# Kernel optimization log

Measured on AMD Instinct MI355X. Metric: run time of the kernel, lower is better.

## Reference

```python
import jax, jax.numpy as jnp
import numpy as np

B, N, DOP, DM, H = 8, 2048, 256, 256, 256  # batch, n_ops==n_machines, dims


def setup_inputs() -> dict:
    key = jax.random.key(0)
    ks = jax.random.split(key, 21)
    s = 0.02
    inp = {
        "operation_features": jax.random.normal(ks[0], (B, N, DOP), jnp.float32),
        "machine_features": jax.random.normal(ks[1], (B, N, DM), jnp.float32),
        "type_match_mask": jax.random.bernoulli(ks[2], 0.3, (B, N, N)).astype(jnp.float32),
        "same_type_mask": jax.random.bernoulli(ks[3], 0.3, (B, N, N)).astype(jnp.float32),
        "oma_q_w": jax.random.normal(ks[4], (H, DM), jnp.float32) * s,
        "oma_q_b": jnp.zeros((H,), jnp.float32),
        "oma_kv_w": jax.random.normal(ks[5], (2 * H, DOP), jnp.float32) * s,
        "oma_kv_b": jnp.zeros((2 * H,), jnp.float32),
        "oma_s_w": jax.random.normal(ks[6], (1, 2 * H), jnp.float32) * s,
        "oma_s_b": jnp.zeros((1,), jnp.float32),
        "oma_o_w": jax.random.normal(ks[7], (DM, H), jnp.float32) * s,
        "oma_o_b": jnp.zeros((DM,), jnp.float32),
        "sa_w_w": jax.random.normal(ks[8], (3 * H, DM), jnp.float32) * s,
        "sa_w_b": jnp.zeros((3 * H,), jnp.float32),
        "sa_s_w": jax.random.normal(ks[9], (1, 2 * H), jnp.float32) * s,
        "sa_s_b": jnp.zeros((1,), jnp.float32),
        "sa_o_w": jax.random.normal(ks[10], (DM, H), jnp.float32) * s,
        "sa_o_b": jnp.zeros((DM,), jnp.float32),
        "mix_w": jax.random.normal(ks[11], (DM, 2 * DM), jnp.float32) * s,
        "mix_b": jnp.zeros((DM,), jnp.float32),
    }
    return inp


def reference(operation_features, machine_features, type_match_mask, same_type_mask,
              oma_q_w, oma_q_b, oma_kv_w, oma_kv_b, oma_s_w, oma_s_b, oma_o_w, oma_o_b,
              sa_w_w, sa_w_b, sa_s_w, sa_s_b, sa_o_w, sa_o_b, mix_w, mix_b):
    # --- OperationMachineAttention ---
    q = machine_features @ oma_q_w.T + oma_q_b            # (B,M,H)
    kv = operation_features @ oma_kv_w.T + oma_kv_b       # (B,C,2H)
    k, v = jnp.split(kv, 2, axis=-1)
    # Linear(cat([q,k])) == q @ W[:, :H].T + k @ W[:, H:].T + b (additive-score factorization)
    sq = jnp.einsum('bmh,h->bm', q, oma_s_w[0, :H])
    sk = jnp.einsum('bch,h->bc', k, oma_s_w[0, H:])
    scores = jax.nn.leaky_relu(sq[:, :, None] + sk[:, None, :] + oma_s_b[0])  # (B,M,C)
    p = jax.nn.softmax(scores * type_match_mask, axis=-1)
    wf = jnp.einsum('bmc,bch->bmh', p, v)
    operation_machine = wf @ oma_o_w.T + oma_o_b           # (B,M,DM)

    # --- SelfAttention over machines ---
    w3 = machine_features @ sa_w_w.T + sa_w_b              # (B,C,3H)
    q2, k2, v2 = jnp.split(w3, 3, axis=-1)
    sq2 = jnp.einsum('bih,h->bi', q2, sa_s_w[0, :H])
    sk2 = jnp.einsum('bjh,h->bj', k2, sa_s_w[0, H:])
    s2 = jax.nn.leaky_relu(sq2[:, :, None] + sk2[:, None, :] + sa_s_b[0])  # (B,C,C)
    p2 = jax.nn.softmax(s2 * same_type_mask, axis=-1)
    machine_machine = jnp.einsum('bij,bjh->bih', p2, v2) @ sa_o_w.T + sa_o_b  # (B,C,DM)

    # --- mix ---
    mixed = jnp.concatenate([operation_machine, machine_machine], axis=-1)
    return mixed @ mix_w.T + mix_b                          # (B,N,DM)
```

## Files before the change

### kernel.cpp

```cpp
#include <hip/hip_runtime.h>
#include <stdint.h>
#include <stddef.h>

#define B_ 8
#define N_ 2048
#define C_ 2048
#define D_ 256
#define H_ 256

typedef __bf16 bf16x8 __attribute__((ext_vector_type(8)));
typedef __bf16 bf16x4 __attribute__((ext_vector_type(4)));
typedef float f32x4 __attribute__((ext_vector_type(4)));

#define MFMA16(a, b, c) __builtin_amdgcn_mfma_f32_16x16x32_bf16((a), (b), (c), 0, 0, 0)

__global__ __launch_bounds__(256) void k0a_partial(
    const float* __restrict__ oma_q_w, const float* __restrict__ oma_kv_w,
    const float* __restrict__ sa_w_w,
    const float* __restrict__ oma_s_w, const float* __restrict__ sa_s_w,
    float* __restrict__ partial)
{
    int d = threadIdx.x;
    int vec = blockIdx.x >> 3, hc = blockIdx.x & 7;
    int h0 = hc * 32;
    const float* Wb; const float* sv;
    if (vec == 0)      { Wb = oma_q_w  + h0 * 256;         sv = oma_s_w + h0; }
    else if (vec == 1) { Wb = oma_kv_w + h0 * 256;         sv = oma_s_w + 256 + h0; }
    else if (vec == 2) { Wb = sa_w_w   + h0 * 256;         sv = sa_s_w + h0; }
    else               { Wb = sa_w_w   + (256 + h0) * 256; sv = sa_s_w + 256 + h0; }
    float a = 0.f;
    #pragma unroll 8
    for (int h = 0; h < 32; ++h) a += Wb[h * 256 + d] * sv[h];
    partial[blockIdx.x * 256 + d] = a;
}

__global__ __launch_bounds__(256) void k0b_reduce(
    const float* __restrict__ partial,
    const float* __restrict__ oma_q_b, const float* __restrict__ oma_kv_b,
    const float* __restrict__ oma_s_w, const float* __restrict__ oma_s_b,
    const float* __restrict__ sa_w_b, const float* __restrict__ sa_s_w,
    const float* __restrict__ sa_s_b,
    float* __restrict__ wq_v, float* __restrict__ wk_v,
    float* __restrict__ wq2_v, float* __restrict__ wk2_v,
    float* __restrict__ sb)
{
    int d = threadIdx.x;
    float a0 = 0.f, a1 = 0.f, a2 = 0.f, a3 = 0.f;
    #pragma unroll
    for (int hc = 0; hc < 8; ++hc) {
        a0 += partial[(0 * 8 + hc) * 256 + d];
        a1 += partial[(1 * 8 + hc) * 256 + d];
        a2 += partial[(2 * 8 + hc) * 256 + d];
        a3 += partial[(3 * 8 + hc) * 256 + d];
    }
    wq_v[d] = a0; wk_v[d] = a1; wq2_v[d] = a2; wk2_v[d] = a3;

    int h = d;
    float p1 = oma_q_b[h] * oma_s_w[h] + oma_kv_b[h] * oma_s_w[256 + h];
    float p2 = sa_w_b[h] * sa_s_w[h] + sa_w_b[256 + h] * sa_s_w[256 + h];
    for (int o = 32; o; o >>= 1) { p1 += __shfl_xor(p1, o); p2 += __shfl_xor(p2, o); }
    __shared__ float redA[4], redB[4];
    int wv = threadIdx.x >> 6;
    if ((threadIdx.x & 63) == 0) { redA[wv] = p1; redB[wv] = p2; }
    __syncthreads();
    if (threadIdx.x == 0) {
        sb[0] = redA[0] + redA[1] + redA[2] + redA[3] + oma_s_b[0];
        sb[1] = redB[0] + redB[1] + redB[2] + redB[3] + sa_s_b[0];
    }
}

__global__ __launch_bounds__(256) void k1_wcat(
    const float* __restrict__ mix_w, const float* __restrict__ mix_b,
    const float* __restrict__ oma_o_w, const float* __restrict__ oma_o_b,
    const float* __restrict__ sa_o_w, const float* __restrict__ sa_o_b,
    __bf16* __restrict__ Wcat, float* __restrict__ b_total)
{
    int d = blockIdx.x, h = threadIdx.x;
    const float* mwr = mix_w + d * 512;
    float w1 = 0.f, w2 = 0.f;
    #pragma unroll 4
    for (int e = 0; e < 256; ++e) {
        w1 += mwr[e] * oma_o_w[e * 256 + h];
        w2 += mwr[256 + e] * sa_o_w[e * 256 + h];
    }
    Wcat[d * 512 + h] = (__bf16)w1;
    Wcat[d * 512 + 256 + h] = (__bf16)w2;

    float pb = mwr[h] * oma_o_b[h] + mwr[256 + h] * sa_o_b[h];
    for (int o = 32; o; o >>= 1) pb += __shfl_xor(pb, o);
    __shared__ float red[4];
    if ((h & 63) == 0) red[h >> 6] = pb;
    __syncthreads();
    if (h == 0) b_total[d] = mix_b[d] + red[0] + red[1] + red[2] + red[3];
}

__global__ __launch_bounds__(256) void k2_scores(
    const float* __restrict__ op, const float* __restrict__ mach,
    const float* __restrict__ wq_v, const float* __restrict__ wk_v,
    const float* __restrict__ wq2_v, const float* __restrict__ wk2_v,
    const float* __restrict__ sb,
    float* __restrict__ sqp, float* __restrict__ skv,
    float* __restrict__ sq2p, float* __restrict__ sk2v)
{
    int t = threadIdx.x, lane = t & 63, wv = t >> 6;
    size_t n = (size_t)blockIdx.x * 4 + wv;
    const float4 mf = *(const float4*)(mach + n * 256 + lane * 4);
    const float4 of = *(const float4*)(op + n * 256 + lane * 4);
    const float4 q4 = *(const float4*)(wq_v + lane * 4);
    const float4 k4 = *(const float4*)(wk_v + lane * 4);
    const float4 q24 = *(const float4*)(wq2_v + lane * 4);
    const float4 k24 = *(const float4*)(wk2_v + lane * 4);
    float s1 = mf.x * q4.x + mf.y * q4.y + mf.z * q4.z + mf.w * q4.w;
    float s2 = of.x * k4.x + of.y * k4.y + of.z * k4.z + of.w * k4.w;
    float s3 = mf.x * q24.x + mf.y * q24.y + mf.z * q24.z + mf.w * q24.w;
    float s4 = mf.x * k24.x + mf.y * k24.y + mf.z * k24.z + mf.w * k24.w;
    for (int o = 32; o; o >>= 1) {
        s1 += __shfl_xor(s1, o); s2 += __shfl_xor(s2, o);
        s3 += __shfl_xor(s3, o); s4 += __shfl_xor(s4, o);
    }
    if (lane == 0) {
        sqp[n] = s1 + sb[0]; skv[n] = s2;
        sq2p[n] = s3 + sb[1]; sk2v[n] = s4;
    }
}

__global__ __launch_bounds__(256, 2) void k3_vgemm(
    const float* __restrict__ op, const float* __restrict__ mach,
    const float* __restrict__ oma_kv_w, const float* __restrict__ sa_w_w,
    __bf16* __restrict__ vt)
{
    __shared__ __attribute__((aligned(16))) __bf16 As[64][72];
    __shared__ __attribute__((aligned(16))) __bf16 Bs[64][72];
    int t = threadIdx.x;
    int bid = blockIdx.x;
    int which = bid >> 10;
    int r = bid & 1023;
    int b = r >> 7;
    int ht = (r >> 5) & 3;
    int ct = r & 31;

    const float* Aglob = (which ? (sa_w_w + 512 * 256) : (oma_kv_w + 256 * 256)) + ht * 64 * 256;
    const float* Bglob = (which ? mach : op) + ((size_t)b * N_ + ct * 64) * 256;

    int lane = t & 63, wv = t >> 6;
    int l15 = lane & 15, qo = (lane >> 4) * 8;
    int rr = t >> 4;
    int dd = (t & 15) * 4;

    f32x4 acc[4] = {};

    for (int d0 = 0; d0 < 256; d0 += 64) {
        #pragma unroll
        for (int p = 0; p < 4; ++p) {
            float4 av = *(const float4*)(Aglob + (size_t)(p * 16 + rr) * 256 + d0 + dd);
            float4 bv = *(const float4*)(Bglob + (size_t)(p * 16 + rr) * 256 + d0 + dd);
            bf16x4 a4, b4;
            a4[0] = (__bf16)av.x; a4[1] = (__bf16)av.y; a4[2] = (__bf16)av.z; a4[3] = (__bf16)av.w;
            b4[0] = (__bf16)bv.x; b4[1] = (__bf16)bv.y; b4[2] = (__bf16)bv.z; b4[3] = (__bf16)bv.w;
            *(bf16x4*)&As[p * 16 + rr][dd] = a4;
            *(bf16x4*)&Bs[p * 16 + rr][dd] = b4;
        }
        __syncthreads();
        #pragma unroll
        for (int kb = 0; kb < 2; ++kb) {
            bf16x8 bfr = *(const bf16x8*)&Bs[16 * wv + l15][kb * 32 + qo];
            #pragma unroll
            for (int rt = 0; rt < 4; ++rt) {
                bf16x8 afr = *(const bf16x8*)&As[16 * rt + l15][kb * 32 + qo];
                acc[rt] = MFMA16(afr, bfr, acc[rt]);
            }
        }
        __syncthreads();
    }
    #pragma unroll
    for (int rt = 0; rt < 4; ++rt)
        #pragma unroll
        for (int j = 0; j < 4; ++j)
            As[16 * rt + (lane >> 4) * 4 + j][16 * wv + l15] = (__bf16)acc[rt][j];
    __syncthreads();
    int hh = t >> 2, cb = (t & 3) * 16;
    __bf16* orow = vt + (((size_t)(which * 8 + b)) * 256 + ht * 64 + hh) * 2048 + ct * 64 + cb;
    *(bf16x8*)(orow) = *(const bf16x8*)&As[hh][cb];
    *(bf16x8*)(orow + 8) = *(const bf16x8*)&As[hh][cb + 8];
}

__device__ __forceinline__ f32x4 ntload4f(const float* p) {
    return __builtin_nontemporal_load(reinterpret_cast<const f32x4*>(p));
}

__global__ __launch_bounds__(256, 2) void k4_attn(
    const float* __restrict__ tmask, const float* __restrict__ smask,
    const float* __restrict__ sqp, const float* __restrict__ skv,
    const float* __restrict__ sq2p, const float* __restrict__ sk2v,
    const __bf16* __restrict__ vt,
    __bf16* __restrict__ wfcat)
{
    __shared__ __attribute__((aligned(16))) __bf16 eA[64][72];
    __shared__ __attribute__((aligned(16))) __bf16 vB[256][72];
    __shared__ uint16_t Mb[64 * 130];
    __shared__ float rowsum[64];

    int t = threadIdx.x;
    int bid = blockIdx.x;
    int wg = (bid & 7) * 64 + (bid >> 3);
    int which = wg >> 8;
    int r = wg & 255;
    int b = r >> 5;
    int m0 = (r & 31) * 64;

    const float* mask = (which ? smask : tmask) + ((size_t)b * N_ + m0) * C_;
    const float* sqrow = (which ? sq2p : sqp) + b * N_ + m0;
    const float* skrow = (which ? sk2v : skv) + b * N_;
    const __bf16* vbase = vt + ((size_t)(which * 8 + b)) * 256 * 2048;

    int lane = t & 63, wv = t >> 6;
    int l15 = lane & 15, qo = (lane >> 4) * 8;
    int mrow = t >> 2;
    int cq16 = (t & 3) * 16;
    int vh = t >> 3;
    int vc = (t & 7) * 8;

    float sqv = sqrow[mrow];
    float psum = 0.f;
    f32x4 acc[4][4] = {};

    bf16x8 vv[8];
    f32x4 skc[4];

    auto load_v = [&](int c0) {
        #pragma unroll
        for (int p = 0; p < 8; ++p)
            vv[p] = *(const bf16x8*)(vbase + (size_t)(p * 32 + vh) * 2048 + c0 + vc);
    };
    auto load_sk = [&](int c0) {
        #pragma unroll
        for (int i = 0; i < 4; ++i) skc[i] = *(const f32x4*)(skrow + c0 + cq16 + 4 * i);
    };

    load_v(0);
    load_sk(0);

    {
        int tcol = t & 127;
        int trow = t >> 7;
        const float* mb = mask + (size_t)trow * C_ + tcol * 16;
        #pragma unroll 4
        for (int i = 0; i < 32; ++i) {
            const float* p = mb + (size_t)i * 2 * C_;
            f32x4 a = ntload4f(p);
            f32x4 bq = ntload4f(p + 4);
            f32x4 cq = ntload4f(p + 8);
            f32x4 dq = ntload4f(p + 12);
            uint32_t bits = 0;
            #pragma unroll
            for (int j = 0; j < 4; ++j) {
                bits |= (a[j]  != 0.f ? 1u : 0u) << j;
                bits |= (bq[j] != 0.f ? 1u : 0u) << (4 + j);
                bits |= (cq[j] != 0.f ? 1u : 0u) << (8 + j);
                bits |= (dq[j] != 0.f ? 1u : 0u) << (12 + j);
            }
            Mb[(i * 2 + trow) * 130 + tcol] = (uint16_t)bits;
        }
    }
    __syncthreads();

    #pragma unroll 1
    for (int c0 = 0; c0 < C_; c0 += 64) {
        #pragma unroll
        for (int p = 0; p < 8; ++p)
            *(bf16x8*)&vB[p * 32 + vh][vc] = vv[p];
        uint32_t mbits = Mb[mrow * 130 + (c0 >> 4) + (t & 3)];
        bf16x8 e0, e1;
        #pragma unroll
        for (int i = 0; i < 16; ++i) {
            float s = sqv + skc[i >> 2][i & 3];
            s = s > 0.f ? s : 0.01f * s;
            float e = (mbits & (1u << i)) ? __expf(s) : 1.0f;
            psum += e;
            if (i < 8) e0[i] = (__bf16)e; else e1[i - 8] = (__bf16)e;
        }
        *(bf16x8*)&eA[mrow][cq16] = e0;
        *(bf16x8*)&eA[mrow][cq16 + 8] = e1;
        __syncthreads();
        int cn = c0 + 64; if (cn >= C_) cn = 0;
        load_v(cn);
        load_sk(cn);
        #pragma unroll
        for (int kb = 0; kb < 2; ++kb) {
            bf16x8 afr[4];
            #pragma unroll
            for (int rt = 0; rt < 4; ++rt)
                afr[rt] = *(const bf16x8*)&eA[16 * rt + l15][kb * 32 + qo];
            #pragma unroll
            for (int ctile = 0; ctile < 4; ++ctile) {
                bf16x8 bfr = *(const bf16x8*)&vB[64 * wv + 16 * ctile + l15][kb * 32 + qo];
                #pragma unroll
                for (int rt = 0; rt < 4; ++rt)
                    acc[rt][ctile] = MFMA16(afr[rt], bfr, acc[rt][ctile]);
            }
        }
        __syncthreads();
    }

    float rs = psum;
    rs += __shfl_xor(rs, 1);
    rs += __shfl_xor(rs, 2);
    if ((t & 3) == 0) rowsum[mrow] = rs;
    __syncthreads();

    __bf16* obuf = &vB[0][0];
    #pragma unroll
    for (int rt = 0; rt < 4; ++rt) {
        #pragma unroll
        for (int j = 0; j < 4; ++j) {
            int m = 16 * rt + (lane >> 4) * 4 + j;
            float inv = __builtin_amdgcn_rcpf(rowsum[m]);
            #pragma unroll
            for (int ctile = 0; ctile < 4; ++ctile)
                obuf[m * 264 + 64 * wv + 16 * ctile + l15] = (__bf16)(acc[rt][ctile][j] * inv);
        }
    }
    __syncthreads();
    int m = t >> 2, cb = (t & 3) * 64;
    __bf16* wrow = wfcat + ((size_t)(b * N_ + m0 + m)) * 512 + which * 256 + cb;
    #pragma unroll
    for (int k = 0; k < 8; ++k)
        *(bf16x8*)(wrow + k * 8) = *(const bf16x8*)&obuf[m * 264 + cb + k * 8];
}

__global__ __launch_bounds__(256, 2) void k5_out(
    const __bf16* __restrict__ wfcat, const __bf16* __restrict__ Wcat,
    const float* __restrict__ b_total, float* __restrict__ out)
{
    __shared__ __attribute__((aligned(16))) __bf16 As[32][72];
    __shared__ __attribute__((aligned(16))) __bf16 Bs[256][72];
    __shared__ float bias[256];
    int t = threadIdx.x;
    int n0 = blockIdx.x * 32;
    int lane = t & 63, wv = t >> 6, l15 = lane & 15, qo = (lane >> 4) * 8;
    bias[t] = b_total[t];
    int ar = t >> 3;
    int ac = (t & 7) * 8;
    f32x4 acc[2][4] = {};

    for (int k0 = 0; k0 < 512; k0 += 64) {
        *(bf16x8*)&As[ar][ac] =
            *(const bf16x8*)(wfcat + (size_t)(n0 + ar) * 512 + k0 + ac);
        #pragma unroll
        for (int p = 0; p < 8; ++p)
            *(bf16x8*)&Bs[p * 32 + ar][ac] =
                *(const bf16x8*)(Wcat + (size_t)(p * 32 + ar) * 512 + k0 + ac);
        __syncthreads();
        #pragma unroll
        for (int kb = 0; kb < 2; ++kb) {
            bf16x8 afr[2];
            #pragma unroll
            for (int rt = 0; rt < 2; ++rt)
                afr[rt] = *(const bf16x8*)&As[16 * rt + l15][kb * 32 + qo];
            #pragma unroll
            for (int ct = 0; ct < 4; ++ct) {
                bf16x8 bfr = *(const bf16x8*)&Bs[64 * wv + 16 * ct + l15][kb * 32 + qo];
                #pragma unroll
                for (int rt = 0; rt < 2; ++rt)
                    acc[rt][ct] = MFMA16(afr[rt], bfr, acc[rt][ct]);
            }
        }
        __syncthreads();
    }
    #pragma unroll
    for (int rt = 0; rt < 2; ++rt) {
        #pragma unroll
        for (int ct = 0; ct < 4; ++ct) {
            int d = 64 * wv + 16 * ct + l15;
            float bv = bias[d];
            #pragma unroll
            for (int j = 0; j < 4; ++j) {
                int m = 16 * rt + (lane >> 4) * 4 + j;
                out[(size_t)(n0 + m) * 256 + d] = acc[rt][ct][j] + bv;
            }
        }
    }
}

extern "C" void kernel_launch(void* const* d_in, const int* in_sizes, int n_in,
                              void* d_out, int out_size, void* d_ws, size_t ws_size,
                              hipStream_t stream)
{
    const float* op_feat  = (const float*)d_in[0];
    const float* mach_feat= (const float*)d_in[1];
    const float* tmask    = (const float*)d_in[2];
    const float* smask    = (const float*)d_in[3];
    const float* oma_q_w  = (const float*)d_in[4];
    const float* oma_q_b  = (const float*)d_in[5];
    const float* oma_kv_w = (const float*)d_in[6];
    const float* oma_kv_b = (const float*)d_in[7];
    const float* oma_s_w  = (const float*)d_in[8];
    const float* oma_s_b  = (const float*)d_in[9];
    const float* oma_o_w  = (const float*)d_in[10];
    const float* oma_o_b  = (const float*)d_in[11];
    const float* sa_w_w   = (const float*)d_in[12];
    const float* sa_w_b   = (const float*)d_in[13];
    const float* sa_s_w   = (const float*)d_in[14];
    const float* sa_s_b   = (const float*)d_in[15];
    const float* sa_o_w   = (const float*)d_in[16];
    const float* sa_o_b   = (const float*)d_in[17];
    const float* mix_w    = (const float*)d_in[18];
    const float* mix_b    = (const float*)d_in[19];

    char* ws = (char*)d_ws;
    float* wq_v   = (float*)(ws + 0);
    float* wk_v   = (float*)(ws + 1024);
    float* wq2_v  = (float*)(ws + 2048);
    float* wk2_v  = (float*)(ws + 3072);
    float* sb     = (float*)(ws + 4096);
    float* btot   = (float*)(ws + 4352);
    float* sqp    = (float*)(ws + 8192);
    float* skv    = (float*)(ws + 73728);
    float* sq2p   = (float*)(ws + 139264);
    float* sk2v   = (float*)(ws + 204800);
    __bf16* Wcat  = (__bf16*)(ws + 270336);
    __bf16* vt    = (__bf16*)(ws + 532480);
    __bf16* wfcat = (__bf16*)(ws + 17309696);
    float* outp   = (float*)d_out;

    float* partial = (float*)(ws + 532480);

    k0a_partial<<<32, 256, 0, stream>>>(oma_q_w, oma_kv_w, sa_w_w,
                                        oma_s_w, sa_s_w, partial);
    k0b_reduce<<<1, 256, 0, stream>>>(partial, oma_q_b, oma_kv_b, oma_s_w, oma_s_b,
                                      sa_w_b, sa_s_w, sa_s_b,
                                      wq_v, wk_v, wq2_v, wk2_v, sb);
    k1_wcat<<<256, 256, 0, stream>>>(mix_w, mix_b, oma_o_w, oma_o_b,
                                     sa_o_w, sa_o_b, Wcat, btot);
    k2_scores<<<4096, 256, 0, stream>>>(op_feat, mach_feat, wq_v, wk_v, wq2_v, wk2_v,
                                        sb, sqp, skv, sq2p, sk2v);
    k3_vgemm<<<2048, 256, 0, stream>>>(op_feat, mach_feat, oma_kv_w, sa_w_w, vt);
    k4_attn<<<512, 256, 0, stream>>>(tmask, smask, sqp, skv, sq2p, sk2v, vt, wfcat);
    k5_out<<<512, 256, 0, stream>>>(wfcat, Wcat, btot, outp);
}
```

Measured before the change: 469.2 us.

## Split attention key dimension across two thread halves with register-resident V fragments

The attention kernel goes from 256 to 512 threads per block. Each half of the block handles half of the key/column range and the two partial accumulators and row sums are combined through shared memory at the end. V tiles are now loaded straight into registers in MFMA operand layout, so V is no longer staged through LDS. The exp tile is double-buffered, which allows one barrier per 64-column step, and the sk scores are preloaded once into LDS. The aim is more waves in flight and less LDS traffic and synchronisation, at the cost of an extra cross-half reduction and higher register pressure.

```diff
diff --git a/kernel.cpp b/kernel.cpp
--- a/kernel.cpp
+++ b/kernel.cpp
@@ -188,17 +188,19 @@
     return __builtin_nontemporal_load(reinterpret_cast<const f32x4*>(p));
 }
 
-__global__ __launch_bounds__(256, 2) void k4_attn(
+__global__ __launch_bounds__(512, 4) void k4_attn(
     const float* __restrict__ tmask, const float* __restrict__ smask,
     const float* __restrict__ sqp, const float* __restrict__ skv,
     const float* __restrict__ sq2p, const float* __restrict__ sk2v,
     const __bf16* __restrict__ vt,
     __bf16* __restrict__ wfcat)
 {
-    __shared__ __attribute__((aligned(16))) __bf16 eA[64][72];
-    __shared__ __attribute__((aligned(16))) __bf16 vB[256][72];
-    __shared__ uint16_t Mb[64 * 130];
-    __shared__ float rowsum[64];
+    __shared__ __attribute__((aligned(16))) unsigned char smem[62208];
+    __bf16* eAll = (__bf16*)smem;
+    uint16_t* Mb = (uint16_t*)(smem + 36864);
+    float* skL = (float*)(smem + 53504);
+    float* rowsumH = (float*)(smem + 61696);
+    float* fbuf = (float*)smem;
 
     int t = threadIdx.x;
     int bid = blockIdx.x;
@@ -213,40 +215,41 @@
     const float* skrow = (which ? sk2v : skv) + b * N_;
     const __bf16* vbase = vt + ((size_t)(which * 8 + b)) * 256 * 2048;
 
-    int lane = t & 63, wv = t >> 6;
+    int half = t >> 8;
+    int tl = t & 255;
+    int lane = tl & 63, wv4 = tl >> 6;
     int l15 = lane & 15, qo = (lane >> 4) * 8;
-    int mrow = t >> 2;
-    int cq16 = (t & 3) * 16;
-    int vh = t >> 3;
-    int vc = (t & 7) * 8;
+    int mrow = tl >> 2;
+    int cq16 = (tl & 3) * 16;
+
+    const __bf16* vptr = vbase + (size_t)(64 * wv4 + l15) * 2048 + half * 1024 + qo;
+    __bf16* eH0 = eAll + (half * 2 + 0) * 4608;
+    __bf16* eH1 = eAll + (half * 2 + 1) * 4608;
 
     float sqv = sqrow[mrow];
     float psum = 0.f;
     f32x4 acc[4][4] = {};
-
     bf16x8 vv[8];
-    f32x4 skc[4];
 
     auto load_v = [&](int c0) {
         #pragma unroll
-        for (int p = 0; p < 8; ++p)
-            vv[p] = *(const bf16x8*)(vbase + (size_t)(p * 32 + vh) * 2048 + c0 + vc);
+        for (int ct = 0; ct < 4; ++ct)
+            #pragma unroll
+            for (int kb = 0; kb < 2; ++kb)
+                vv[ct * 2 + kb] = *(const bf16x8*)(vptr + (size_t)ct * 16 * 2048 + c0 + kb * 32);
     };
-    auto load_sk = [&](int c0) {
-        #pragma unroll
-        for (int i = 0; i < 4; ++i) skc[i] = *(const f32x4*)(skrow + c0 + cq16 + 4 * i);
-    };
 
     load_v(0);
-    load_sk(0);
+    *(f32x4*)(skL + t * 4) = *(const f32x4*)(skrow + t * 4);
 
     {
-        int tcol = t & 127;
-        int trow = t >> 7;
-        const float* mb = mask + (size_t)trow * C_ + tcol * 16;
+        int col16 = t & 127;
+        int rg = t >> 7;
+        const float* mp = mask + (size_t)rg * C_ + col16 * 16;
+        uint16_t* mbp = Mb + rg * 130 + col16;
         #pragma unroll 4
-        for (int i = 0; i < 32; ++i) {
-            const float* p = mb + (size_t)i * 2 * C_;
+        for (int i = 0; i < 16; ++i) {
+            const float* p = mp + (size_t)i * 4 * C_;
             f32x4 a = ntload4f(p);
             f32x4 bq = ntload4f(p + 4);
             f32x4 cq = ntload4f(p + 8);
@@ -259,73 +262,119 @@
                 bits |= (cq[j] != 0.f ? 1u : 0u) << (8 + j);
                 bits |= (dq[j] != 0.f ? 1u : 0u) << (12 + j);
             }
-            Mb[(i * 2 + trow) * 130 + tcol] = (uint16_t)bits;
+            mbp[i * 4 * 130] = (uint16_t)bits;
         }
     }
     __syncthreads();
 
-    #pragma unroll 1
-    for (int c0 = 0; c0 < C_; c0 += 64) {
-        #pragma unroll
-        for (int p = 0; p < 8; ++p)
-            *(bf16x8*)&vB[p * 32 + vh][vc] = vv[p];
-        uint32_t mbits = Mb[mrow * 130 + (c0 >> 4) + (t & 3)];
+    const float* skLp = skL + half * 1024 + cq16;
+    const uint16_t* mbq = Mb + mrow * 130 + half * 64 + (tl & 3);
+
+    auto compute_e = [&](int c0, __bf16* eb) {
+        uint32_t mbits = mbq[c0 >> 4];
+        f32x4 sk0 = *(const f32x4*)(skLp + c0);
+        f32x4 sk1 = *(const f32x4*)(skLp + c0 + 4);
+        f32x4 sk2 = *(const f32x4*)(skLp + c0 + 8);
+        f32x4 sk3 = *(const f32x4*)(skLp + c0 + 12);
+        float sk[16];
+        #pragma unroll
+        for (int j = 0; j < 4; ++j) {
+            sk[j] = sk0[j]; sk[4 + j] = sk1[j]; sk[8 + j] = sk2[j]; sk[12 + j] = sk3[j];
+        }
         bf16x8 e0, e1;
         #pragma unroll
         for (int i = 0; i < 16; ++i) {
-            float s = sqv + skc[i >> 2][i & 3];
+            float s = sqv + sk[i];
             s = s > 0.f ? s : 0.01f * s;
             float e = (mbits & (1u << i)) ? __expf(s) : 1.0f;
             psum += e;
             if (i < 8) e0[i] = (__bf16)e; else e1[i - 8] = (__bf16)e;
         }
-        *(bf16x8*)&eA[mrow][cq16] = e0;
-        *(bf16x8*)&eA[mrow][cq16 + 8] = e1;
-        __syncthreads();
-        int cn = c0 + 64; if (cn >= C_) cn = 0;
-        load_v(cn);
-        load_sk(cn);
+        *(bf16x8*)&eb[mrow * 72 + cq16] = e0;
+        *(bf16x8*)&eb[mrow * 72 + cq16 + 8] = e1;
+    };
+    auto do_mfma = [&](const __bf16* eb) {
         #pragma unroll
         for (int kb = 0; kb < 2; ++kb) {
             bf16x8 afr[4];
             #pragma unroll
             for (int rt = 0; rt < 4; ++rt)
-                afr[rt] = *(const bf16x8*)&eA[16 * rt + l15][kb * 32 + qo];
-            #pragma unroll
-            for (int ctile = 0; ctile < 4; ++ctile) {
-                bf16x8 bfr = *(const bf16x8*)&vB[64 * wv + 16 * ctile + l15][kb * 32 + qo];
+                afr[rt] = *(const bf16x8*)&eb[(16 * rt + l15) * 72 + kb * 32 + qo];
+            #pragma unroll
+            for (int ct = 0; ct < 4; ++ct)
                 #pragma unroll
                 for (int rt = 0; rt < 4; ++rt)
-                    acc[rt][ctile] = MFMA16(afr[rt], bfr, acc[rt][ctile]);
-            }
-        }
-        __syncthreads();
+                    acc[rt][ct] = MFMA16(afr[rt], vv[ct * 2 + kb], acc[rt][ct]);
+        }
+    };
+
+    #pragma unroll 1
+    for (int it = 0; it < 8; ++it) {
+        int cE = it * 128, cO = cE + 64;
+        compute_e(cE, eH0);
+        asm volatile("s_waitcnt lgkmcnt(0)" ::: "memory");
+        __builtin_amdgcn_s_barrier();
+        do_mfma(eH0);
+        load_v(cO);
+        compute_e(cO, eH1);
+        asm volatile("s_waitcnt lgkmcnt(0)" ::: "memory");
+        __builtin_amdgcn_s_barrier();
+        do_mfma(eH1);
+        load_v((cE + 128) & 1023);
     }
 
     float rs = psum;
     rs += __shfl_xor(rs, 1);
     rs += __shfl_xor(rs, 2);
-    if ((t & 3) == 0) rowsum[mrow] = rs;
+    if ((tl & 3) == 0) rowsumH[half * 64 + mrow] = rs;
     __syncthreads();
 
-    __bf16* obuf = &vB[0][0];
     #pragma unroll
-    for (int rt = 0; rt < 4; ++rt) {
-        #pragma unroll
-        for (int j = 0; j < 4; ++j) {
-            int m = 16 * rt + (lane >> 4) * 4 + j;
-            float inv = __builtin_amdgcn_rcpf(rowsum[m]);
-            #pragma unroll
-            for (int ctile = 0; ctile < 4; ++ctile)
-                obuf[m * 264 + 64 * wv + 16 * ctile + l15] = (__bf16)(acc[rt][ctile][j] * inv);
-        }
-    }
-    __syncthreads();
-    int m = t >> 2, cb = (t & 3) * 64;
-    __bf16* wrow = wfcat + ((size_t)(b * N_ + m0 + m)) * 512 + which * 256 + cb;
-    #pragma unroll
-    for (int k = 0; k < 8; ++k)
-        *(bf16x8*)(wrow + k * 8) = *(const bf16x8*)&obuf[m * 264 + cb + k * 8];
+    for (int p = 0; p < 2; ++p) {
+        if (half == 1) {
+            #pragma unroll
+            for (int rr2 = 0; rr2 < 2; ++rr2) {
+                int rt = 2 * p + rr2;
+                #pragma unroll
+                for (int ct = 0; ct < 4; ++ct)
+                    #pragma unroll
+                    for (int j = 0; j < 4; ++j) {
+                        int ml = 16 * rr2 + (lane >> 4) * 4 + j;
+                        fbuf[ml * 260 + 64 * wv4 + 16 * ct + l15] = acc[rt][ct][j];
+                    }
+            }
+        }
+        __syncthreads();
+        if (half == 0) {
+            #pragma unroll
+            for (int rr2 = 0; rr2 < 2; ++rr2) {
+                int rt = 2 * p + rr2;
+                #pragma unroll
+                for (int j = 0; j < 4; ++j) {
+                    int ml = 16 * rr2 + (lane >> 4) * 4 + j;
+                    int m = 32 * p + ml;
+                    float inv = __builtin_amdgcn_rcpf(rowsumH[m] + rowsumH[64 + m]);
+                    #pragma unroll
+                    for (int ct = 0; ct < 4; ++ct) {
+                        int cc = 64 * wv4 + 16 * ct + l15;
+                        fbuf[ml * 260 + cc] = (acc[rt][ct][j] + fbuf[ml * 260 + cc]) * inv;
+                    }
+                }
+            }
+        }
+        __syncthreads();
+        {
+            int row = t >> 4, c16 = (t & 15) * 16;
+            const float* fr = fbuf + row * 260 + c16;
+            bf16x8 o0, o1;
+            #pragma unroll
+            for (int k = 0; k < 8; ++k) { o0[k] = (__bf16)fr[k]; o1[k] = (__bf16)fr[8 + k]; }
+            __bf16* wrow = wfcat + ((size_t)(b * N_ + m0 + 32 * p + row)) * 512 + which * 256 + c16;
+            *(bf16x8*)wrow = o0;
+            *(bf16x8*)(wrow + 8) = o1;
+        }
+        __syncthreads();
+    }
 }
 
 __global__ __launch_bounds__(256, 2) void k5_out(
@@ -435,6 +484,6 @@
     k2_scores<<<4096, 256, 0, stream>>>(op_feat, mach_feat, wq_v, wk_v, wq2_v, wk2_v,
                                         sb, sqp, skv, sq2p, sk2v);
     k3_vgemm<<<2048, 256, 0, stream>>>(op_feat, mach_feat, oma_kv_w, sa_w_w, vt);
-    k4_attn<<<512, 256, 0, stream>>>(tmask, smask, sqp, skv, sq2p, sk2v, vt, wfcat);
+    k4_attn<<<512, 512, 0, stream>>>(tmask, smask, sqp, skv, sq2p, sk2v, vt, wfcat);
     k5_out<<<512, 256, 0, stream>>>(wfcat, Wcat, btot, outp);
 }
```

Result: slower. 506.7 us (+8.0%).
